# Performance work log

Measured on AMD Instinct MI355X. Metric: run time of the kernel, lower is better.

## Reference

```python
import jax, jax.numpy as jnp
import numpy as np

B, T, F, H = 1024, 128, 64, 256
HH = H // 2
A = 2  # action_space_size


def setup_inputs() -> dict:
    key = jax.random.key(0)
    ks = jax.random.split(key, 16)
    s = 0.05
    return {
        "history": jax.random.normal(ks[0], (B, T, F), jnp.float32),
        "head": jax.random.normal(ks[1], (B, 3), jnp.float32),
        # peephole LSTM params (TF LSTMCell gate order: i, j, f, o)
        "kernel": jax.random.normal(ks[2], (F + H, 4 * H), jnp.float32) * s,
        "bias": jnp.zeros((4 * H,), jnp.float32),
        "w_i": jax.random.normal(ks[3], (H,), jnp.float32) * s,
        "w_f": jax.random.normal(ks[4], (H,), jnp.float32) * s,
        "w_o": jax.random.normal(ks[5], (H,), jnp.float32) * s,
        # dueling heads
        "fc3_w": jax.random.normal(ks[6], (H + 2, HH), jnp.float32) * s,
        "fc3_b": jnp.zeros((HH,), jnp.float32),
        "fc4_w": jax.random.normal(ks[7], (H + 2, HH), jnp.float32) * s,
        "fc4_b": jnp.zeros((HH,), jnp.float32),
        "sell_v_w": jax.random.normal(ks[8], (HH, 1), jnp.float32) * s,
        "sell_v_b": jnp.zeros((1,), jnp.float32),
        "sell_q_w": jax.random.normal(ks[9], (HH, A), jnp.float32) * s,
        "sell_q_b": jnp.zeros((A,), jnp.float32),
        "buy_v_w": jax.random.normal(ks[10], (HH, 1), jnp.float32) * s,
        "buy_v_b": jnp.zeros((1,), jnp.float32),
        "buy_q_w": jax.random.normal(ks[11], (HH, A), jnp.float32) * s,
        "buy_q_b": jnp.zeros((A,), jnp.float32),
    }


def _peephole_lstm(history, kernel, bias, w_i, w_f, w_o):
    # history: [B, T, F] -> final hidden state h: [B, H]
    b = history.shape[0]
    h_dim = w_i.shape[0]
    xs = jnp.swapaxes(history, 0, 1)  # [T, B, F] time-major for scan
    c0 = jnp.zeros((b, h_dim), history.dtype)
    h0 = jnp.zeros((b, h_dim), history.dtype)

    def step(carry, x_t):
        c, h = carry
        z = jnp.concatenate([x_t, h], axis=-1) @ kernel + bias  # [B, 4H]
        i, j, f, o = jnp.split(z, 4, axis=-1)
        i = jax.nn.sigmoid(i + w_i * c)
        f = jax.nn.sigmoid(f + 1.0 + w_f * c)  # forget_bias = 1.0 (TF default)
        c_new = f * c + i * jnp.tanh(j)
        o = jax.nn.sigmoid(o + w_o * c_new)
        h_new = o * jnp.tanh(c_new)
        return (c_new, h_new), None

    (c_fin, h_fin), _ = jax.lax.scan(step, (c0, h0), xs)
    return h_fin


def reference(history, head, kernel, bias, w_i, w_f, w_o,
              fc3_w, fc3_b, fc4_w, fc4_b,
              sell_v_w, sell_v_b, sell_q_w, sell_q_b,
              buy_v_w, buy_v_b, buy_q_w, buy_q_b):
    state = _peephole_lstm(history, kernel, bias, w_i, w_f, w_o)  # [B, H]
    is_pos = head[:, :1]   # [B, 1]
    net_pnl = head[:, 1:]  # [B, 2]
    feature = jnp.concatenate([net_pnl, state], axis=-1)  # [B, H+2]

    value_logits = jax.nn.relu(feature @ fc3_w + fc3_b)
    q_logits = jax.nn.relu(feature @ fc4_w + fc4_b)

    pos_adv = q_logits @ sell_q_w + sell_q_b
    pos_q = pos_adv - jnp.mean(pos_adv, axis=-1, keepdims=True) + (value_logits @ sell_v_w + sell_v_b)
    emp_adv = q_logits @ buy_q_w + buy_q_b
    emp_q = emp_adv - jnp.mean(emp_adv, axis=-1, keepdims=True) + (value_logits @ buy_v_w + buy_v_b)

    mask = jnp.concatenate([is_pos, 1.0 - is_pos], axis=1).astype(bool)  # [B, 2]
    q = jnp.where(mask, pos_q, emp_q)
    return q
```

## Files before the change

### kernel.cpp

```cpp
#include <hip/hip_runtime.h>
#include <stdint.h>

#define B_TOTAL 1024
#define T_STEPS 128
#define F_DIM   64
#define H_DIM   256
#define BROWS   16
#define APAD    324
#define NSLOTS  640

typedef float f32x4 __attribute__((ext_vector_type(4)));
typedef short bf16x8 __attribute__((ext_vector_type(8)));

__device__ __forceinline__ unsigned short f2bf(float f) {
  unsigned int u = __float_as_uint(f);
  u += 0x7fffu + ((u >> 16) & 1u);
  return (unsigned short)(u >> 16);
}
__device__ __forceinline__ float bf2f(unsigned short b) {
  return __uint_as_float(((unsigned int)b) << 16);
}
__device__ __forceinline__ float sigmoid_f(float x) {
  return 1.0f / (1.0f + __expf(-x));
}
__device__ __forceinline__ float tanh_f(float x) {
  return 1.0f - 2.0f / (1.0f + __expf(2.0f * x));
}

__global__ __launch_bounds__(64) void pack_w_kernel(const float* __restrict__ W,
                                                    unsigned short* __restrict__ Wp) {
  const int slot = blockIdx.x;
  const int w  = slot / 80, r = slot % 80;
  const int kt = r >> 3, ct = (r >> 2) & 1, g = r & 3;
  const int ntile = g * 16 + w * 2 + ct;
  const int l   = threadIdx.x;
  const int col = ntile * 16 + (l & 15);
  const int k0  = kt * 32 + (l >> 4) * 8;
  unsigned short* dst = Wp + ((size_t)slot * 64 + l) * 8;
  #pragma unroll
  for (int j = 0; j < 8; ++j)
    dst[j] = f2bf(W[(size_t)(k0 + j) * 1024 + col]);
}

#define PIN_V(x) asm volatile("" : "+v"(x))
#define PIN_A(x) asm volatile("" : "+a"(x))

#define ISSUE_BATCH(buf, kt, ct) do {                                        \
    const unsigned short* _p = wp_wl + ((kt) * 8 + (ct) * 4) * 512;          \
    asm volatile("global_load_dwordx4 %0, %4, off\n\t"                       \
                 "global_load_dwordx4 %1, %4, off offset:1024\n\t"           \
                 "global_load_dwordx4 %2, %4, off offset:2048\n\t"           \
                 "global_load_dwordx4 %3, %4, off offset:3072"               \
                 : "=&v"(buf[0]), "=&v"(buf[1]), "=&v"(buf[2]), "=&v"(buf[3])\
                 : "v"(_p));                                                 \
  } while (0)

#define CONSUME_S(buf, ct, afv, N) do {                                      \
    asm volatile("s_waitcnt vmcnt(" #N ")" ::: "memory");                    \
    __builtin_amdgcn_sched_barrier(0);                                       \
    acc[ct][0] = __builtin_amdgcn_mfma_f32_16x16x32_bf16(afv, buf[0], acc[ct][0], 0, 0, 0); \
    acc[ct][1] = __builtin_amdgcn_mfma_f32_16x16x32_bf16(afv, buf[1], acc[ct][1], 0, 0, 0); \
    acc[ct][2] = __builtin_amdgcn_mfma_f32_16x16x32_bf16(afv, buf[2], acc[ct][2], 0, 0, 0); \
    acc[ct][3] = __builtin_amdgcn_mfma_f32_16x16x32_bf16(afv, buf[3], acc[ct][3], 0, 0, 0); \
    __builtin_amdgcn_sched_barrier(0);                                       \
  } while (0)

#define LD_A(kt) (*(const bf16x8*)&A_lds[cl][(kt) * 32 + kg * 8])

__global__ __launch_bounds__(512, 1) void qlstm_kernel(
    const float* __restrict__ history, const float* __restrict__ head,
    const float* __restrict__ bias,
    const float* __restrict__ w_i, const float* __restrict__ w_f, const float* __restrict__ w_o,
    const unsigned short* __restrict__ Wp,
    const float* __restrict__ fc3_w, const float* __restrict__ fc3_b,
    const float* __restrict__ fc4_w, const float* __restrict__ fc4_b,
    const float* __restrict__ sell_v_w, const float* __restrict__ sell_v_b,
    const float* __restrict__ sell_q_w, const float* __restrict__ sell_q_b,
    const float* __restrict__ buy_v_w, const float* __restrict__ buy_v_b,
    const float* __restrict__ buy_q_w, const float* __restrict__ buy_q_b,
    float* __restrict__ out) {

  __shared__ unsigned short A_lds[BROWS][APAD];
  __shared__ unsigned short W_lds[128 * 512];

  const int tid = threadIdx.x;
  const int w   = tid >> 6;
  const int l   = tid & 63;
  const int cl  = l & 15;
  const int kg  = l >> 4;
  const int rb  = blockIdx.x * BROWS;

  const unsigned short* wp_wl = Wp + (size_t)(w * 80) * 512 + l * 8;
  const unsigned short* wl_l  = W_lds + (w * 16) * 512 + l * 8;

  for (int i = tid; i < 128 * 64; i += 512) {
    const int s = i >> 6, l2 = i & 63;
    const int fsrc = (s >> 4) * 80 + 32 + (s & 15);
    *(uint4*)&W_lds[((size_t)s * 64 + l2) * 8] =
        *(const uint4*)&Wp[((size_t)fsrc * 64 + l2) * 8];
  }

  bf16x8 wreg[4][2][4];
  #pragma unroll
  for (int kt = 0; kt < 4; ++kt)
    #pragma unroll
    for (int ct = 0; ct < 2; ++ct)
      #pragma unroll
      for (int g = 0; g < 4; ++g) {
        wreg[kt][ct][g] = *(const bf16x8*)(wp_wl + (kt * 8 + ct * 4 + g) * 512);
        if (kt < 3) PIN_A(wreg[kt][ct][g]); else PIN_V(wreg[kt][ct][g]);
      }

  for (int i = tid; i < BROWS * APAD; i += 512)
    ((unsigned short*)A_lds)[i] = 0;
  __syncthreads();
  {
    const int r  = tid >> 5;
    const int f0 = (tid & 31) * 2;
    const float2 xv0 = *(const float2*)&history[((size_t)(rb + r) * T_STEPS + 0) * F_DIM + f0];
    *(unsigned int*)&A_lds[r][f0] =
        (unsigned int)f2bf(xv0.x) | ((unsigned int)f2bf(xv0.y) << 16);
  }

  float bias_r[2][4], wi_r[2], wf_r[2], wo_r[2];
  #pragma unroll
  for (int ct = 0; ct < 2; ++ct) {
    const int hc = (w * 2 + ct) * 16 + cl;
    wi_r[ct] = w_i[hc]; wf_r[ct] = w_f[hc]; wo_r[ct] = w_o[hc];
    #pragma unroll
    for (int g = 0; g < 4; ++g) bias_r[ct][g] = bias[g * 256 + hc];
  }

  float c_st[2][4];
  #pragma unroll
  for (int ct = 0; ct < 2; ++ct)
    #pragma unroll
    for (int q = 0; q < 4; ++q) c_st[ct][q] = 0.0f;

  __syncthreads();

  for (int t = 0; t < T_STEPS; ++t) {
    float2 xv;
    const bool havex = (t + 1 < T_STEPS);
    if (havex) {
      const float* xp =
          &history[((size_t)(rb + (tid >> 5)) * T_STEPS + (t + 1)) * F_DIM + (tid & 31) * 2];
      asm volatile("global_load_dwordx2 %0, %1, off" : "=&v"(xv) : "v"(xp));
    }

    f32x4 acc[2][4];
    #pragma unroll
    for (int ct = 0; ct < 2; ++ct)
      #pragma unroll
      for (int g = 0; g < 4; ++g)
        acc[ct][g] = (f32x4){0.f, 0.f, 0.f, 0.f};

    bf16x8 sA[4], sB[4];
    ISSUE_BATCH(sA, 6, 0);
    ISSUE_BATCH(sB, 6, 1);

    #pragma unroll
    for (int kt = 0; kt < 4; ++kt) {
      const bf16x8 afr = LD_A(kt);
      #pragma unroll
      for (int ct = 0; ct < 2; ++ct)
        #pragma unroll
        for (int g = 0; g < 4; ++g)
          acc[ct][g] =
              __builtin_amdgcn_mfma_f32_16x16x32_bf16(afr, wreg[kt][ct][g], acc[ct][g], 0, 0, 0);
    }

    #pragma unroll
    for (int kt = 4; kt < 6; ++kt) {
      const bf16x8 afr = LD_A(kt);
      #pragma unroll
      for (int ct = 0; ct < 2; ++ct)
        #pragma unroll
        for (int g = 0; g < 4; ++g) {
          const bf16x8 b = *(const bf16x8*)(wl_l + ((kt - 4) * 8 + ct * 4 + g) * 512);
          acc[ct][g] = __builtin_amdgcn_mfma_f32_16x16x32_bf16(afr, b, acc[ct][g], 0, 0, 0);
        }
    }

    bf16x8 af;
    af = LD_A(6);
    CONSUME_S(sA, 0, af, 4); ISSUE_BATCH(sA, 7, 0);
    CONSUME_S(sB, 1, af, 4); ISSUE_BATCH(sB, 7, 1);
    af = LD_A(7);
    CONSUME_S(sA, 0, af, 4); ISSUE_BATCH(sA, 8, 0);
    CONSUME_S(sB, 1, af, 4); ISSUE_BATCH(sB, 8, 1);
    af = LD_A(8);
    CONSUME_S(sA, 0, af, 4); ISSUE_BATCH(sA, 9, 0);
    CONSUME_S(sB, 1, af, 4); ISSUE_BATCH(sB, 9, 1);
    af = LD_A(9);
    CONSUME_S(sA, 0, af, 4);
    CONSUME_S(sB, 1, af, 0);

    float h_val[2][4];
    #pragma unroll
    for (int ct = 0; ct < 2; ++ct) {
      #pragma unroll
      for (int q = 0; q < 4; ++q) {
        const float c_old = c_st[ct][q];
        const float ig = sigmoid_f(acc[ct][0][q] + bias_r[ct][0] + wi_r[ct] * c_old);
        const float fg = sigmoid_f(acc[ct][2][q] + bias_r[ct][2] + 1.0f + wf_r[ct] * c_old);
        const float jg = tanh_f(acc[ct][1][q] + bias_r[ct][1]);
        const float c_new = fg * c_old + ig * jg;
        const float og = sigmoid_f(acc[ct][3][q] + bias_r[ct][3] + wo_r[ct] * c_new);
        c_st[ct][q] = c_new;
        h_val[ct][q] = og * tanh_f(c_new);
      }
    }

    __syncthreads();

    #pragma unroll
    for (int ct = 0; ct < 2; ++ct) {
      const int hc = (w * 2 + ct) * 16 + cl;
      #pragma unroll
      for (int q = 0; q < 4; ++q)
        A_lds[4 * kg + q][64 + hc] = f2bf(h_val[ct][q]);
    }
    if (havex) {
      const int r  = tid >> 5;
      const int f0 = (tid & 31) * 2;
      *(unsigned int*)&A_lds[r][f0] =
          (unsigned int)f2bf(xv.x) | ((unsigned int)f2bf(xv.y) << 16);
    }
    __syncthreads();
  }

  asm volatile("s_waitcnt vmcnt(0)" ::: "memory");
  __builtin_amdgcn_sched_barrier(0);
  __syncthreads();

  float* feat  = (float*)W_lds;
  float* v_l   = feat + BROWS * 258;
  float* q_l   = v_l + BROWS * 128;
  float* ispos = q_l + BROWS * 128;

  for (int i = tid; i < BROWS * H_DIM; i += 512) {
    const int r = i >> 8, hc = i & 255;
    feat[r * 258 + 2 + hc] = bf2f(A_lds[r][64 + hc]);
  }
  if (tid < BROWS) {
    feat[tid * 258 + 0] = head[(rb + tid) * 3 + 1];
    feat[tid * 258 + 1] = head[(rb + tid) * 3 + 2];
    ispos[tid] = head[(rb + tid) * 3 + 0];
  }
  __syncthreads();

  #pragma unroll
  for (int p = 0; p < 4; ++p) {
    const int idx = p * 512 + tid;
    const int r = idx >> 7, hh = idx & 127;
    float s3 = fc3_b[hh], s4 = fc4_b[hh];
    for (int k = 0; k < 258; ++k) {
      const float fv = feat[r * 258 + k];
      s3 += fv * fc3_w[k * 128 + hh];
      s4 += fv * fc4_w[k * 128 + hh];
    }
    v_l[r * 128 + hh] = fmaxf(s3, 0.0f);
    q_l[r * 128 + hh] = fmaxf(s4, 0.0f);
  }
  __syncthreads();

  if (tid < BROWS) {
    const int r = tid;
    float pa0 = sell_q_b[0], pa1 = sell_q_b[1];
    float ea0 = buy_q_b[0],  ea1 = buy_q_b[1];
    float sv = sell_v_b[0], bv = buy_v_b[0];
    for (int hh = 0; hh < 128; ++hh) {
      const float qv = q_l[r * 128 + hh], vv = v_l[r * 128 + hh];
      pa0 += qv * sell_q_w[hh * 2 + 0];
      pa1 += qv * sell_q_w[hh * 2 + 1];
      ea0 += qv * buy_q_w[hh * 2 + 0];
      ea1 += qv * buy_q_w[hh * 2 + 1];
      sv += vv * sell_v_w[hh];
      bv += vv * buy_v_w[hh];
    }
    const float pm = 0.5f * (pa0 + pa1), em = 0.5f * (ea0 + ea1);
    const float pq0 = pa0 - pm + sv, pq1 = pa1 - pm + sv;
    const float eq0 = ea0 - em + bv, eq1 = ea1 - em + bv;
    const float ip = ispos[r];
    out[(size_t)(rb + r) * 2 + 0] = (ip != 0.0f) ? pq0 : eq0;
    out[(size_t)(rb + r) * 2 + 1] = ((1.0f - ip) != 0.0f) ? pq1 : eq1;
  }
}

extern "C" void kernel_launch(void* const* d_in, const int* in_sizes, int n_in,
                              void* d_out, int out_size, void* d_ws, size_t ws_size,
                              hipStream_t stream) {
  (void)in_sizes; (void)n_in; (void)out_size; (void)ws_size;
  const float* history  = (const float*)d_in[0];
  const float* head     = (const float*)d_in[1];
  const float* Wk       = (const float*)d_in[2];
  const float* bias     = (const float*)d_in[3];
  const float* w_i      = (const float*)d_in[4];
  const float* w_f      = (const float*)d_in[5];
  const float* w_o      = (const float*)d_in[6];
  const float* fc3_w    = (const float*)d_in[7];
  const float* fc3_b    = (const float*)d_in[8];
  const float* fc4_w    = (const float*)d_in[9];
  const float* fc4_b    = (const float*)d_in[10];
  const float* sell_v_w = (const float*)d_in[11];
  const float* sell_v_b = (const float*)d_in[12];
  const float* sell_q_w = (const float*)d_in[13];
  const float* sell_q_b = (const float*)d_in[14];
  const float* buy_v_w  = (const float*)d_in[15];
  const float* buy_v_b  = (const float*)d_in[16];
  const float* buy_q_w  = (const float*)d_in[17];
  const float* buy_q_b  = (const float*)d_in[18];

  unsigned short* Wp = (unsigned short*)d_ws;

  pack_w_kernel<<<NSLOTS, 64, 0, stream>>>(Wk, Wp);
  qlstm_kernel<<<B_TOTAL / BROWS, 512, 0, stream>>>(
      history, head, bias, w_i, w_f, w_o, Wp,
      fc3_w, fc3_b, fc4_w, fc4_b,
      sell_v_w, sell_v_b, sell_q_w, sell_q_b,
      buy_v_w, buy_v_b, buy_q_w, buy_q_b,
      (float*)d_out);
}
```

Before: 746.8 us.

## Double-buffer LSTM activation tile and deepen streamed weight prefetch

Splits the shared activation tile into two buffers indexed by step parity. Each step reads the current buffer and writes the new hidden state and the next input into the other, which removes one block-wide barrier per timestep. It also keeps a third batch of global weight loads in flight, rotating three register buffers with looser waitcnt thresholds, to hide more load latency. The costs are extra LDS and VGPR usage and more complex wait-count bookkeeping.

```diff
diff --git a/kernel.cpp b/kernel.cpp
--- a/kernel.cpp
+++ b/kernel.cpp
@@ -65,7 +65,7 @@
     __builtin_amdgcn_sched_barrier(0);                                       \
   } while (0)
 
-#define LD_A(kt) (*(const bf16x8*)&A_lds[cl][(kt) * 32 + kg * 8])
+#define LD_A(buf, kt) (*(const bf16x8*)&(buf)[cl][(kt) * 32 + kg * 8])
 
 __global__ __launch_bounds__(512, 1) void qlstm_kernel(
     const float* __restrict__ history, const float* __restrict__ head,
@@ -80,7 +80,7 @@
     const float* __restrict__ buy_q_w, const float* __restrict__ buy_q_b,
     float* __restrict__ out) {
 
-  __shared__ unsigned short A_lds[BROWS][APAD];
+  __shared__ unsigned short A_lds[2][BROWS][APAD];
   __shared__ unsigned short W_lds[128 * 512];
 
   const int tid = threadIdx.x;
@@ -112,13 +112,13 @@
       }
 
   for (int i = tid; i < BROWS * APAD; i += 512)
-    ((unsigned short*)A_lds)[i] = 0;
+    ((unsigned short*)A_lds[0])[i] = 0;
   __syncthreads();
   {
     const int r  = tid >> 5;
     const int f0 = (tid & 31) * 2;
     const float2 xv0 = *(const float2*)&history[((size_t)(rb + r) * T_STEPS + 0) * F_DIM + f0];
-    *(unsigned int*)&A_lds[r][f0] =
+    *(unsigned int*)&A_lds[0][r][f0] =
         (unsigned int)f2bf(xv0.x) | ((unsigned int)f2bf(xv0.y) << 16);
   }
 
@@ -140,6 +140,9 @@
   __syncthreads();
 
   for (int t = 0; t < T_STEPS; ++t) {
+    unsigned short (*Acur)[APAD] = A_lds[t & 1];
+    unsigned short (*Anxt)[APAD] = A_lds[(t + 1) & 1];
+
     float2 xv;
     const bool havex = (t + 1 < T_STEPS);
     if (havex) {
@@ -155,13 +158,14 @@
       for (int g = 0; g < 4; ++g)
         acc[ct][g] = (f32x4){0.f, 0.f, 0.f, 0.f};
 
-    bf16x8 sA[4], sB[4];
+    bf16x8 sA[4], sB[4], sC[4];
     ISSUE_BATCH(sA, 6, 0);
     ISSUE_BATCH(sB, 6, 1);
+    ISSUE_BATCH(sC, 7, 0);
 
     #pragma unroll
     for (int kt = 0; kt < 4; ++kt) {
-      const bf16x8 afr = LD_A(kt);
+      const bf16x8 afr = LD_A(Acur, kt);
       #pragma unroll
       for (int ct = 0; ct < 2; ++ct)
         #pragma unroll
@@ -172,7 +176,7 @@
 
     #pragma unroll
     for (int kt = 4; kt < 6; ++kt) {
-      const bf16x8 afr = LD_A(kt);
+      const bf16x8 afr = LD_A(Acur, kt);
       #pragma unroll
       for (int ct = 0; ct < 2; ++ct)
         #pragma unroll
@@ -183,16 +187,16 @@
     }
 
     bf16x8 af;
-    af = LD_A(6);
-    CONSUME_S(sA, 0, af, 4); ISSUE_BATCH(sA, 7, 0);
-    CONSUME_S(sB, 1, af, 4); ISSUE_BATCH(sB, 7, 1);
-    af = LD_A(7);
-    CONSUME_S(sA, 0, af, 4); ISSUE_BATCH(sA, 8, 0);
-    CONSUME_S(sB, 1, af, 4); ISSUE_BATCH(sB, 8, 1);
-    af = LD_A(8);
-    CONSUME_S(sA, 0, af, 4); ISSUE_BATCH(sA, 9, 0);
-    CONSUME_S(sB, 1, af, 4); ISSUE_BATCH(sB, 9, 1);
-    af = LD_A(9);
+    af = LD_A(Acur, 6);
+    CONSUME_S(sA, 0, af, 8); ISSUE_BATCH(sA, 7, 1);
+    CONSUME_S(sB, 1, af, 8); ISSUE_BATCH(sB, 8, 0);
+    af = LD_A(Acur, 7);
+    CONSUME_S(sC, 0, af, 8); ISSUE_BATCH(sC, 8, 1);
+    CONSUME_S(sA, 1, af, 8); ISSUE_BATCH(sA, 9, 0);
+    af = LD_A(Acur, 8);
+    CONSUME_S(sB, 0, af, 8); ISSUE_BATCH(sB, 9, 1);
+    CONSUME_S(sC, 1, af, 8);
+    af = LD_A(Acur, 9);
     CONSUME_S(sA, 0, af, 4);
     CONSUME_S(sB, 1, af, 0);
 
@@ -212,19 +216,17 @@
       }
     }
 
-    __syncthreads();
-
     #pragma unroll
     for (int ct = 0; ct < 2; ++ct) {
       const int hc = (w * 2 + ct) * 16 + cl;
       #pragma unroll
       for (int q = 0; q < 4; ++q)
-        A_lds[4 * kg + q][64 + hc] = f2bf(h_val[ct][q]);
+        Anxt[4 * kg + q][64 + hc] = f2bf(h_val[ct][q]);
     }
     if (havex) {
       const int r  = tid >> 5;
       const int f0 = (tid & 31) * 2;
-      *(unsigned int*)&A_lds[r][f0] =
+      *(unsigned int*)&Anxt[r][f0] =
           (unsigned int)f2bf(xv.x) | ((unsigned int)f2bf(xv.y) << 16);
     }
     __syncthreads();
@@ -241,7 +243,7 @@
 
   for (int i = tid; i < BROWS * H_DIM; i += 512) {
     const int r = i >> 8, hc = i & 255;
-    feat[r * 258 + 2 + hc] = bf2f(A_lds[r][64 + hc]);
+    feat[r * 258 + 2 + hc] = bf2f(A_lds[0][r][64 + hc]);
   }
   if (tid < BROWS) {
     feat[tid * 258 + 0] = head[(rb + tid) * 3 + 1];
```

Measured after the change: 1.015 ms. 1.36x slower.
